# Optimization experiments

Measured on AMD Instinct MI355X. Metric: run time of the kernel, lower is better.

Reference implementation:

```python
import jax, jax.numpy as jnp
import numpy as np

TRACK_SIZE = 16
# 8 variable-length sequences; sum = 131072 total tokens
LENGTHS = np.array([8192, 16384, 32768, 4096, 24576, 12288, 2048, 30720], dtype=np.int64)
D_MODEL = 256  # n_tracks = 16 tracks of size 16


def setup_inputs() -> dict:
    key = jax.random.key(0)
    T = int(LENGTHS.sum())
    x = jax.random.normal(key, (T, D_MODEL), dtype=jnp.float32)
    lengths = jnp.asarray(LENGTHS)
    return {"x": x, "lengths": lengths}


def reference(x, lengths):
    # x: [T, D] flat ragged batch; lengths: [B] segment lengths summing to T.
    # Track i (i>=1) is circularly rolled by -2^(i-1) within each segment,
    # i.e. out[j, track i] = x[start + (pos_j + 2^(i-1)) % len, track i].
    T, D = x.shape
    ts = TRACK_SIZE
    n_tracks = D // ts
    B = lengths.shape[0]

    cs = jnp.cumsum(lengths)
    starts = jnp.concatenate([jnp.zeros((1,), lengths.dtype), cs[:-1]])  # [B]
    seq_id = jnp.repeat(jnp.arange(B), lengths, total_repeat_length=T)    # [T]
    tok_start = starts[seq_id]                                            # [T]
    tok_len = lengths[seq_id]                                             # [T]
    pos = jnp.arange(T) - tok_start                                       # position within segment

    # shift for track 0 is 0, track i is 2^(i-1)
    shifts = jnp.array([0] + [2 ** (i - 1) for i in range(1, n_tracks)], dtype=lengths.dtype)  # [n_tracks]
    src_pos = (pos[:, None] + shifts[None, :]) % tok_len[:, None]         # [T, n_tracks]
    src = tok_start[:, None] + src_pos                                    # global source row per track

    x3 = x.reshape(T, n_tracks, ts)
    z = jnp.take_along_axis(x3, src[:, :, None], axis=0)                  # fused gather over all tracks
    return z.reshape(T, D)
```

## Files before the change

kernel.cpp:

```cpp
#include <hip/hip_runtime.h>
#include <hip/hip_bf16.h>


typedef float f32x4 __attribute__((ext_vector_type(4)));

__global__ __launch_bounds__(256) void
rotate_chord_kernel(const float* __restrict__ x,
                    const int* __restrict__ lengths,
                    float* __restrict__ out,
                    int T, int B) {
    int wave  = threadIdx.x >> 6;
    int lane  = threadIdx.x & 63;
    int track = lane >> 2;
    int quad  = lane & 3;
    int t0    = blockIdx.x * 8 + wave;
    if (t0 >= T) return;

    unsigned shift = (track == 0) ? 0u : (1u << (track - 1));
    int col = track * 16 + quad * 4;

    size_t srcoff[2];
#pragma unroll
    for (int k = 0; k < 2; ++k) {
        int t = t0 + 4 * k;
        int start = 0, len = 1, acc = 0;
        for (int b = 0; b < B; ++b) {
            int L = lengths[b];
            if (t >= acc) { start = acc; len = L; }
            acc += L;
        }
        unsigned sp = (unsigned)(t - start) + shift;
        sp -= (sp / (unsigned)len) * (unsigned)len;
        srcoff[k] = (size_t)(start + (int)sp) * 256 + col;
    }

    bool has2 = (t0 + 4) < T;
    f32x4 v0 = *reinterpret_cast<const f32x4*>(x + srcoff[0]);
    f32x4 v1 = has2 ? *reinterpret_cast<const f32x4*>(x + srcoff[1]) : v0;

    *reinterpret_cast<f32x4*>(out + (size_t)t0 * 256 + lane * 4) = v0;
    if (has2)
        *reinterpret_cast<f32x4*>(out + (size_t)(t0 + 4) * 256 + lane * 4) = v1;
}

extern "C" void kernel_launch(void* const* d_in, const int* in_sizes, int n_in,
                              void* d_out, int out_size, void* d_ws, size_t ws_size,
                              hipStream_t stream) {
    const float* x       = (const float*)d_in[0];
    const int*   lengths = (const int*)d_in[1];
    float*       out     = (float*)d_out;

    const int D = 256;
    int T = in_sizes[0] / D;
    int B = in_sizes[1];

    int blocks = (T + 7) / 8;

    rotate_chord_kernel<<<blocks, 256, 0, stream>>>(x, lengths, out, T, B);
}
```

Baseline: 49.90 us.

## Process 16 contiguous rows per wave with incremental source position

After: 53.28 us. +6.8%, slower.

```diff
diff --git a/kernel.cpp b/kernel.cpp
--- a/kernel.cpp
+++ b/kernel.cpp
@@ -4,43 +4,66 @@
 
 typedef float f32x4 __attribute__((ext_vector_type(4)));
 
-__global__ __launch_bounds__(256) void
+#define CHUNK 16
+
+__global__ __launch_bounds__(256, 8) void
 rotate_chord_kernel(const float* __restrict__ x,
                     const int* __restrict__ lengths,
                     float* __restrict__ out,
                     int T, int B) {
-    int wave  = threadIdx.x >> 6;
+    int wave  = (blockIdx.x * blockDim.x + threadIdx.x) >> 6;
     int lane  = threadIdx.x & 63;
     int track = lane >> 2;
     int quad  = lane & 3;
-    int t0    = blockIdx.x * 8 + wave;
-    if (t0 >= T) return;
+
+    int t_begin = wave * CHUNK;
+    if (t_begin >= T) return;
+    int t_end = t_begin + CHUNK;
+    if (t_end > T) t_end = T;
 
     unsigned shift = (track == 0) ? 0u : (1u << (track - 1));
     int col = track * 16 + quad * 4;
 
-    size_t srcoff[2];
-#pragma unroll
-    for (int k = 0; k < 2; ++k) {
-        int t = t0 + 4 * k;
-        int start = 0, len = 1, acc = 0;
-        for (int b = 0; b < B; ++b) {
-            int L = lengths[b];
-            if (t >= acc) { start = acc; len = L; }
-            acc += L;
+    int start = 0, len = 1, acc = 0;
+    for (int b = 0; b < B; ++b) {
+        int L = lengths[b];
+        if (t_begin >= acc) { start = acc; len = L; }
+        acc += L;
+    }
+    unsigned sp = (unsigned)(t_begin - start) + shift;
+    sp -= (sp / (unsigned)len) * (unsigned)len;
+
+    const float* __restrict__ xs = x + col;
+    float* __restrict__ os = out + lane * 4;
+
+    if (t_end <= start + len && t_end == t_begin + CHUNK) {
+        size_t obase = (size_t)t_begin * 256;
+#pragma unroll 4
+        for (int i = 0; i < CHUNK; ++i) {
+            f32x4 v = *reinterpret_cast<const f32x4*>(
+                xs + (size_t)(start + (int)sp) * 256);
+            *reinterpret_cast<f32x4*>(os + obase + (size_t)i * 256) = v;
+            sp = (sp + 1 == (unsigned)len) ? 0u : sp + 1;
         }
-        unsigned sp = (unsigned)(t - start) + shift;
-        sp -= (sp / (unsigned)len) * (unsigned)len;
-        srcoff[k] = (size_t)(start + (int)sp) * 256 + col;
+    } else {
+        for (int t = t_begin; t < t_end; ++t) {
+            if (t >= start + len) {
+                int s2 = 0, l2 = 1, a2 = 0;
+                for (int b = 0; b < B; ++b) {
+                    int L = lengths[b];
+                    if (t >= a2) { s2 = a2; l2 = L; }
+                    a2 += L;
+                }
+                start = s2; len = l2;
+                sp = (unsigned)(t - start) + shift;
+                sp -= (sp / (unsigned)len) * (unsigned)len;
+            }
+            f32x4 v = *reinterpret_cast<const f32x4*>(
+                xs + (size_t)(start + (int)sp) * 256);
+            *reinterpret_cast<f32x4*>(os + (size_t)t * 256) = v;
+            sp = (sp + 1 == (unsigned)len) ? 0u : sp + 1;
+        }
     }
-
-    bool has2 = (t0 + 4) < T;
-    f32x4 v0 = *reinterpret_cast<const f32x4*>(x + srcoff[0]);
-    f32x4 v1 = has2 ? *reinterpret_cast<const f32x4*>(x + srcoff[1]) : v0;
-
-    *reinterpret_cast<f32x4*>(out + (size_t)t0 * 256 + lane * 4) = v0;
-    if (has2)
-        *reinterpret_cast<f32x4*>(out + (size_t)(t0 + 4) * 256 + lane * 4) = v1;
 }
 
 extern "C" void kernel_launch(void* const* d_in, const int* in_sizes, int n_in,
@@ -54,7 +77,7 @@
     int T = in_sizes[0] / D;
     int B = in_sizes[1];
 
-    int blocks = (T + 7) / 8;
+    int blocks = (T + 4 * CHUNK - 1) / (4 * CHUNK);
 
     rotate_chord_kernel<<<blocks, 256, 0, stream>>>(x, lengths, out, T, B);
 }
```
